# Kernel tuning notes

Measured on AMD Instinct MI355X. Metric: run time of the kernel, lower is better.

Reference implementation:

```python
import jax, jax.numpy as jnp
import numpy as np
from jax import lax

INV_SQRT2 = np.float32(1.0 / np.sqrt(2.0))

def conv2d(x, w, b=None, stride=1, pad=0):
    y = lax.conv_general_dilated(x, w, (stride, stride), [(pad, pad), (pad, pad)],
                                 dimension_numbers=('NCHW', 'OIHW', 'NCHW'))
    return y if b is None else y + b[None, :, None, None]

def haar_dwt2_zero(x):
    # pytorch_wavelets DWTForward(J=1, wave='haar', mode='zero') for odd H,W:
    # pad one zero at the end of each spatial dim, then pairwise Haar analysis.
    x = jnp.pad(x, ((0, 0), (0, 0), (0, 1), (0, 1)))
    xe, xo = x[..., 0::2], x[..., 1::2]
    lo_w, hi_w = (xe + xo) * INV_SQRT2, (xe - xo) * INV_SQRT2
    def rows(t):
        te, to = t[:, :, 0::2, :], t[:, :, 1::2, :]
        return (te + to) * INV_SQRT2, (te - to) * INV_SQRT2
    ll, lh = rows(lo_w)
    hl, hh = rows(hi_w)
    return ll, lh, hl, hh  # cA, cH, cV, cD

def pixel_shuffle2(x):
    B, C, H, W = x.shape
    co = C // 4
    return x.reshape(B, co, 2, 2, H, W).transpose(0, 1, 4, 2, 5, 3).reshape(B, co, H * 2, W * 2)

def gaussian_kernel5(sigma=0.5):
    r = np.arange(5, dtype=np.float64) - 2.0
    k = np.exp(-(r ** 2) / (2.0 * sigma * sigma))
    return jnp.asarray((k / k.sum()).astype(np.float32))

_GK = gaussian_kernel5(0.5)

def gaussian_blur5(x4d):
    # cv2.GaussianBlur ksize=(5,5) sigma=0.5, default BORDER_REFLECT_101 -> 'reflect' pad
    p = jnp.pad(x4d, ((0, 0), (0, 0), (2, 2), (2, 2)), mode='reflect')
    p = conv2d(p, _GK.reshape(1, 1, 5, 1))
    return conv2d(p, _GK.reshape(1, 1, 1, 5))

def channel_attention(x, w1, w2):
    avg = jnp.mean(x, axis=(2, 3), keepdims=True)
    mx = jnp.max(x, axis=(2, 3), keepdims=True)
    mlp = lambda v: conv2d(jax.nn.relu(conv2d(v, w1)), w2)
    return jax.nn.sigmoid(mlp(avg) + mlp(mx)) * x

def _forward(x, w_x1, b_x1, w_x2, b_x2, w_x3, b_x3, w_hi, b_hi, w_lo, b_lo,
             ca1_w1, ca1_w2, ca2_w1, ca2_w2, w_cat, b_cat, w_c9a, b_c9a, w_c9b, b_c9b):
    f1 = jax.nn.relu(conv2d(x, w_x1, b_x1))            # (1,16,H,W)
    f2 = jax.nn.relu(conv2d(f1, w_x2, b_x2))           # (1,8,H,W)
    tmp12 = jax.nn.relu(conv2d(f2, w_x3, b_x3))        # (1,1,H,W)
    cA, cH, cV, cD = haar_dwt2_zero(tmp12)             # each (1,1,(H+1)/2,(W+1)/2)
    hf = pixel_shuffle2(jax.nn.relu(conv2d(jnp.concatenate([cH, cV, cD], 1), w_hi, b_hi, pad=1)))
    lf = pixel_shuffle2(jax.nn.relu(conv2d(cA, w_lo, b_lo, pad=1)))  # (1,1,H+5,W+5)
    # original detaches hf (cpu->numpy->cv2->cuda): gradients do not flow through it
    hf = gaussian_blur5(lax.stop_gradient(hf))
    hf = channel_attention(hf, ca1_w1, ca1_w2)
    lf = channel_attention(lf, ca2_w1, ca2_w2)
    alpha = 1.0
    cat = jax.nn.relu(conv2d(jnp.concatenate([alpha * hf, (1.0 - alpha) * lf], 1), w_cat, b_cat))
    f12 = tmp12 + cat                                   # (1,1,H,W)
    h = jax.nn.relu(conv2d(f12, w_c9a, b_c9a, pad=1))   # (1,32,H,W)
    return jax.nn.relu(conv2d(h, w_c9b, b_c9b, pad=1))  # (1,64,H,W)

def setup_inputs() -> dict:
    key = jax.random.key(0)
    ks = jax.random.split(key, 24)
    f32 = jnp.float32
    n = lambda k, s, sc=0.05: jax.random.normal(k, s, f32) * sc
    H = W = 511
    return {
        'x': jax.random.normal(ks[0], (1, 204, H, W), f32),
        'w_x1': n(ks[1], (16, 204, 1, 1)), 'b_x1': n(ks[2], (16,)),
        'w_x2': n(ks[3], (8, 16, 1, 1)),   'b_x2': n(ks[4], (8,)),
        'w_x3': n(ks[5], (1, 8, 1, 1)),    'b_x3': n(ks[6], (1,)),
        'w_hi': n(ks[7], (4, 3, 1, 1)),    'b_hi': n(ks[8], (4,)),
        'w_lo': n(ks[9], (4, 1, 1, 1)),    'b_lo': n(ks[10], (4,)),
        'ca1_w1': n(ks[11], (1, 1, 1, 1), 0.5), 'ca1_w2': n(ks[12], (1, 1, 1, 1), 0.5),
        'ca2_w1': n(ks[13], (1, 1, 1, 1), 0.5), 'ca2_w2': n(ks[14], (1, 1, 1, 1), 0.5),
        'w_cat': n(ks[15], (1, 2, 6, 6)),  'b_cat': n(ks[16], (1,)),
        'w_c9a': n(ks[17], (32, 1, 3, 3)), 'b_c9a': n(ks[18], (32,)),
        'w_c9b': n(ks[19], (64, 32, 3, 3)), 'b_c9b': n(ks[20], (64,)),
    }

def reference(x, w_x1, b_x1, w_x2, b_x2, w_x3, b_x3, w_hi, b_hi, w_lo, b_lo,
              ca1_w1, ca1_w2, ca2_w1, ca2_w2, w_cat, b_cat, w_c9a, b_c9a, w_c9b, b_c9b):
    return _forward(x, w_x1, b_x1, w_x2, b_x2, w_x3, b_x3, w_hi, b_hi, w_lo, b_lo,
                    ca1_w1, ca1_w2, ca2_w1, ca2_w2, w_cat, b_cat, w_c9a, b_c9a, w_c9b, b_c9b)
```

## Files before the change

kernel.cpp:

```cpp
#include <hip/hip_runtime.h>
#include <hip/hip_bf16.h>
#include <math.h>

#define NP    261121
#define SPB   512
#define RS    520
#define OFS   16640
#define WPX   520
#define ROWN  4160
#define PSTR  2138240
#define NBP   289

typedef __attribute__((ext_vector_type(8))) short short8;
typedef __attribute__((ext_vector_type(4))) short short4v;
typedef __attribute__((ext_vector_type(4))) float f32x4;
typedef __attribute__((ext_vector_type(4), aligned(4))) float f32x4a;

static __device__ __forceinline__ unsigned short f2bf(float f) {
    unsigned int u = __builtin_bit_cast(unsigned int, f);
    u += 0x7FFFu + ((u >> 16) & 1u);
    return (unsigned short)(u >> 16);
}

static __device__ __forceinline__ short bf16s(float f) {
    __hip_bfloat16 h = __float2bfloat16(f);
    return __builtin_bit_cast(short, h);
}

__global__ __launch_bounds__(256, 2) void k_conv123(const float* __restrict__ x,
                                                    const float* __restrict__ w_x1,
                                                    const float* __restrict__ b1,
                                                    const float* __restrict__ w2,
                                                    const float* __restrict__ b2,
                                                    const float* __restrict__ w3,
                                                    const float* __restrict__ b3,
                                                    const float* __restrict__ w_c9b,
                                                    float* __restrict__ tmp12,
                                                    unsigned short* __restrict__ wb2,
                                                    unsigned short* __restrict__ h2)
{
    {
        int t = blockIdx.x * 256 + threadIdx.x;
        if (t < 18432) {
            int o = t / 288, ck = t - o * 288;
            int c = ck / 9, k = ck - c * 9;
            wb2[k * 2048 + o * 32 + c] = f2bf(w_c9b[t]);
        }
        short8 z8 = {0, 0, 0, 0, 0, 0, 0, 0};
        if (t < 4160) {
            int pl = t / 1040;
            int rr = t - pl * 1040;
            int row = rr >= 520 ? 512 : 0;
            int ch  = rr >= 520 ? rr - 520 : rr;
            *reinterpret_cast<short8*>(h2 + (size_t)pl * PSTR + (size_t)row * ROWN + ch * 8) = z8;
        }
        int z = t - 4160;
        if (z >= 0 && z < 6132) {
            int row = z / 12 + 1;
            int j = z - (row - 1) * 12;
            int pl = j / 3, cidx = j - pl * 3;
            int col = (cidx == 0) ? 0 : (cidx == 1 ? 512 : 513);
            *reinterpret_cast<short8*>(h2 + (size_t)pl * PSTR + (size_t)row * ROWN + col * 8) = z8;
        }
    }

    __shared__ unsigned short sb[2 * OFS];

    const int tid = threadIdx.x;
    const int v = tid >> 6, l = tid & 63;
    const int lpx = l & 15, kg = l >> 4;
    int pxb = blockIdx.x * SPB;
    if (pxb > NP - SPB) pxb = NP - SPB;

    short8 afr[7];
    {
        const float* wrow = w_x1 + lpx * 204;
#pragma unroll
        for (int ks = 0; ks < 7; ++ks)
#pragma unroll
            for (int j = 0; j < 8; ++j) {
                int c = ks * 32 + kg * 8 + j;
                afr[ks][j] = (short)f2bf(c < 204 ? wrow[c] : 0.f);
            }
    }

    const float* xb = x + pxb + 4 * l;
    const float* lpB[8];
#pragma unroll
    for (int i = 0; i < 8; ++i)
        lpB[i] = xb + (size_t)(v * 8 + i) * NP;

    f32x4 acc[8];
#pragma unroll
    for (int n = 0; n < 8; ++n) acc[n] = (f32x4){0.f, 0.f, 0.f, 0.f};

    f32x4a q0[8], q1[8];

#define LOADISSUE(KS) do { \
        _Pragma("unroll") \
        for (int i = 0; i < 8; ++i) { \
            const float* p = ((KS) < 6 || v * 8 + i < 12) ? lpB[i] + (size_t)(KS) * 32 * NP : xb; \
            q0[i] = *reinterpret_cast<const f32x4a*>(p); \
            q1[i] = *reinterpret_cast<const f32x4a*>(p + 256); \
        } \
    } while (0)

#define CVTWRITE(BUF) do { \
        _Pragma("unroll") \
        for (int i = 0; i < 8; ++i) { \
            unsigned short* row = sb + (BUF) * OFS + (v * 8 + i) * RS; \
            short4v w0, w1; \
            _Pragma("unroll") \
            for (int n = 0; n < 4; ++n) { w0[n] = bf16s(q0[i][n]); w1[n] = bf16s(q1[i][n]); } \
            *reinterpret_cast<short4v*>(row + 4 * l)       = w0; \
            *reinterpret_cast<short4v*>(row + 256 + 4 * l) = w1; \
        } \
    } while (0)

#define COMPUTE(KS, BUF) do { \
        short8 r0, r1, r2, r3, r4, r5, r6, r7; \
        const unsigned short* base = sb + (BUF) * OFS + kg * 8 * RS + v * 128 + lpx * 8; \
        r0 = *reinterpret_cast<const short8*>(base); \
        r1 = *reinterpret_cast<const short8*>(base + RS); \
        r2 = *reinterpret_cast<const short8*>(base + 2 * RS); \
        r3 = *reinterpret_cast<const short8*>(base + 3 * RS); \
        r4 = *reinterpret_cast<const short8*>(base + 4 * RS); \
        r5 = *reinterpret_cast<const short8*>(base + 5 * RS); \
        r6 = *reinterpret_cast<const short8*>(base + 6 * RS); \
        r7 = *reinterpret_cast<const short8*>(base + 7 * RS); \
        _Pragma("unroll") \
        for (int n = 0; n < 8; ++n) { \
            short8 b; \
            b[0] = r0[n]; b[1] = r1[n]; b[2] = r2[n]; b[3] = r3[n]; \
            b[4] = r4[n]; b[5] = r5[n]; b[6] = r6[n]; b[7] = r7[n]; \
            acc[n] = __builtin_amdgcn_mfma_f32_16x16x32_bf16(afr[KS], b, acc[n], 0, 0, 0); \
        } \
    } while (0)

    LOADISSUE(0);
    CVTWRITE(0);

#define STEP(K, LAST) do { \
        if (!(LAST)) LOADISSUE((K) + 1); \
        __syncthreads(); \
        COMPUTE((K), (K) & 1); \
        if (!(LAST)) CVTWRITE(((K) + 1) & 1); \
    } while (0)

    STEP(0, 0); STEP(1, 0); STEP(2, 0); STEP(3, 0); STEP(4, 0); STEP(5, 0); STEP(6, 1);
#undef LOADISSUE
#undef CVTWRITE
#undef COMPUTE
#undef STEP

    float4 b1v = *reinterpret_cast<const float4*>(b1 + kg * 4);
    float4 w2v[8];
#pragma unroll
    for (int j = 0; j < 8; ++j)
        w2v[j] = *reinterpret_cast<const float4*>(w2 + j * 16 + kg * 4);
    float b2v[8], w3v[8];
#pragma unroll
    for (int j = 0; j < 8; ++j) { b2v[j] = b2[j]; w3v[j] = w3[j]; }
    float b3v = b3[0];

    f32x4 rlo, rhi;
#pragma unroll
    for (int n = 0; n < 8; ++n) {
        float f0 = fmaxf(acc[n][0] + b1v.x, 0.f);
        float f1 = fmaxf(acc[n][1] + b1v.y, 0.f);
        float f2 = fmaxf(acc[n][2] + b1v.z, 0.f);
        float f3 = fmaxf(acc[n][3] + b1v.w, 0.f);
        float tmp = b3v;
#pragma unroll
        for (int j = 0; j < 8; ++j) {
            float sj = f0 * w2v[j].x;
            sj = fmaf(f1, w2v[j].y, sj);
            sj = fmaf(f2, w2v[j].z, sj);
            sj = fmaf(f3, w2v[j].w, sj);
            sj += __shfl_xor(sj, 16, 64);
            sj += __shfl_xor(sj, 32, 64);
            tmp = fmaf(fmaxf(sj + b2v[j], 0.f), w3v[j], tmp);
        }
        if (n < 4) rlo[n] = fmaxf(tmp, 0.f);
        else       rhi[n - 4] = fmaxf(tmp, 0.f);
    }
    if (kg == 0) {
        float* dst = tmp12 + pxb + v * 128 + lpx * 8;
        *reinterpret_cast<f32x4a*>(dst)     = rlo;
        *reinterpret_cast<f32x4a*>(dst + 4) = rhi;
    }
}

__global__ __launch_bounds__(256) void k_dwtblur(const float* __restrict__ tmp12,
                                                 const float* __restrict__ w_hi,
                                                 const float* __restrict__ b_hi,
                                                 float* __restrict__ hfb,
                                                 float* __restrict__ psum,
                                                 float* __restrict__ pmax,
                                                 float g0, float g1, float g2)
{
    __shared__ float hfT[36][37];
    __shared__ float ss[256], sm[256];
    const float INV = 0.70710678118654752440f;

    int tid = threadIdx.x;
    int bx = blockIdx.x % 17, by = blockIdx.x / 17;
    int X0 = bx * 32, Y0 = by * 32;
    int Ylo = Y0 - 2 < 0 ? 0 : Y0 - 2;
    int Yhi = Y0 + 33 > 515 ? 515 : Y0 + 33;
    int Xlo = X0 - 2 < 0 ? 0 : X0 - 2;
    int Xhi = X0 + 33 > 515 ? 515 : X0 + 33;
    int hlo = Ylo >> 1, hhi = Yhi >> 1, nh = hhi - hlo + 1;
    int wlo = Xlo >> 1, whi = Xhi >> 1, nw = whi - wlo + 1;
    int ncells = nh * nw;

    float wh[12], bh[4];
#pragma unroll
    for (int i = 0; i < 12; ++i) wh[i] = w_hi[i];
#pragma unroll
    for (int o = 0; o < 4; ++o) bh[o] = b_hi[o];

    for (int ci = tid; ci < ncells; ci += 256) {
        int h = hlo + ci / nw, w = wlo + ci % nw;
        float v[4];
        if (h == 0 || h == 257 || w == 0 || w == 257) {
#pragma unroll
            for (int o = 0; o < 4; ++o) v[o] = fmaxf(bh[o], 0.f);
        } else {
            int hh = h - 1, ww = w - 1;
            int r0 = 2 * hh, r1 = 2 * hh + 1, c0 = 2 * ww, c1 = 2 * ww + 1;
            float a = tmp12[r0 * 511 + c0];
            float b = (c1 < 511) ? tmp12[r0 * 511 + c1] : 0.f;
            float c = (r1 < 511) ? tmp12[r1 * 511 + c0] : 0.f;
            float d = (r1 < 511 && c1 < 511) ? tmp12[r1 * 511 + c1] : 0.f;
            float lo0 = (a + b) * INV, hi0 = (a - b) * INV;
            float lo1 = (c + d) * INV, hi1 = (c - d) * INV;
            float cH = (lo0 - lo1) * INV;
            float cV = (hi0 + hi1) * INV;
            float cD = (hi0 - hi1) * INV;
#pragma unroll
            for (int o = 0; o < 4; ++o)
                v[o] = fmaxf(wh[o * 3 + 0] * cH + wh[o * 3 + 1] * cV + wh[o * 3 + 2] * cD + bh[o], 0.f);
        }
#pragma unroll
        for (int dy = 0; dy < 2; ++dy)
#pragma unroll
            for (int dx = 0; dx < 2; ++dx) {
                int Y = 2 * h + dy, X = 2 * w + dx;
                if (Y >= Ylo && Y <= Yhi && X >= Xlo && X <= Xhi)
                    hfT[Y - Y0 + 2][X - X0 + 2] = v[dy * 2 + dx];
            }
    }
    __syncthreads();

    float g[5] = {g0, g1, g2, g1, g0};
    float lsum = 0.f, lmax = -3.4e38f;
#pragma unroll
    for (int k2 = 0; k2 < 4; ++k2) {
        int o = tid + k2 * 256;
        int oy = o >> 5, ox = o & 31;
        int gy = Y0 + oy, gx = X0 + ox;
        if (gy < 516 && gx < 516) {
            int ly[5], lx[5];
#pragma unroll
            for (int i = 0; i < 5; ++i) {
                int yy = gy + i - 2; yy = yy < 0 ? -yy : (yy > 515 ? 1030 - yy : yy);
                int xx = gx + i - 2; xx = xx < 0 ? -xx : (xx > 515 ? 1030 - xx : xx);
                ly[i] = yy - Y0 + 2; lx[i] = xx - X0 + 2;
            }
            float s = 0.f;
#pragma unroll
            for (int i = 0; i < 5; ++i) {
                float rs = 0.f;
#pragma unroll
                for (int j = 0; j < 5; ++j) rs = fmaf(g[j], hfT[ly[i]][lx[j]], rs);
                s = fmaf(g[i], rs, s);
            }
            hfb[gy * 516 + gx] = s;
            lsum += s; lmax = fmaxf(lmax, s);
        }
    }

    ss[tid] = lsum; sm[tid] = lmax;
    __syncthreads();
    for (int off = 128; off > 0; off >>= 1) {
        if (tid < off) { ss[tid] += ss[tid + off]; sm[tid] = fmaxf(sm[tid], sm[tid + off]); }
        __syncthreads();
    }
    if (tid == 0) { psum[blockIdx.x] = ss[0]; pmax[blockIdx.x] = sm[0]; }
}

__global__ __launch_bounds__(256) void k_catc9a(const float* __restrict__ hfb,
                                                const float* __restrict__ tmp12,
                                                const float* __restrict__ psum,
                                                const float* __restrict__ pmax,
                                                const float* __restrict__ caw1,
                                                const float* __restrict__ caw2,
                                                const float* __restrict__ w_cat,
                                                const float* __restrict__ b_cat,
                                                const float* __restrict__ w_c9a,
                                                const float* __restrict__ bias9a,
                                                unsigned short* __restrict__ h2)
{
    __shared__ float f12T[18][19];
    __shared__ float ss[256], sm[256];
    __shared__ float ssc;
    int tid = threadIdx.x;

    {
        float s = 0.f, m = -3.4e38f;
        for (int i = tid; i < NBP; i += 256) { s += psum[i]; m = fmaxf(m, pmax[i]); }
        ss[tid] = s; sm[tid] = m;
        __syncthreads();
        for (int off = 128; off > 0; off >>= 1) {
            if (tid < off) { ss[tid] += ss[tid + off]; sm[tid] = fmaxf(sm[tid], sm[tid + off]); }
            __syncthreads();
        }
        if (tid == 0) {
            float avg = ss[0] / 266256.f;
            float a = caw1[0], b = caw2[0];
            float z = b * fmaxf(a * avg, 0.f) + b * fmaxf(a * sm[0], 0.f);
            ssc = 1.f / (1.f + expf(-z));
        }
        __syncthreads();
    }
    float sc = ssc;

    int tx0 = (blockIdx.x & 31) * 16, ty0 = (blockIdx.x >> 5) * 16;

    for (int idx = tid; idx < 324; idx += 256) {
        int r = idx / 18, c = idx - 18 * r;
        int fy = ty0 - 1 + r, fx = tx0 - 1 + c;
        float val = 0.f;
        if (fy >= 0 && fy < 511 && fx >= 0 && fx < 511) {
            float a6 = 0.f;
#pragma unroll
            for (int ky = 0; ky < 6; ++ky) {
                const float* row = hfb + (fy + ky) * 516 + fx;
#pragma unroll
                for (int kx = 0; kx < 6; ++kx) a6 = fmaf(row[kx], w_cat[ky * 6 + kx], a6);
            }
            val = tmp12[fy * 511 + fx] + fmaxf(sc * a6 + b_cat[0], 0.f);
        }
        f12T[r][c] = val;
    }
    __syncthreads();

    int lr = tid >> 4, lc = tid & 15;
    int oy = ty0 + lr, ox = tx0 + lc;
    if (oy >= 511 || ox >= 511) return;

    float hv[9];
#pragma unroll
    for (int ky = 0; ky < 3; ++ky)
#pragma unroll
        for (int kx = 0; kx < 3; ++kx)
            hv[ky * 3 + kx] = f12T[lr + ky][lc + kx];

    float acc[32];
#pragma unroll
    for (int o = 0; o < 32; ++o) acc[o] = bias9a[o];
#pragma unroll
    for (int k = 0; k < 9; ++k) {
        float v = hv[k];
#pragma unroll
        for (int o = 0; o < 32; ++o) acc[o] = fmaf(v, w_c9a[o * 9 + k], acc[o]);
    }
    unsigned short o16[32];
#pragma unroll
    for (int o = 0; o < 32; ++o) o16[o] = f2bf(fmaxf(acc[o], 0.f));
    size_t px = (size_t)(oy + 1) * WPX + (ox + 1);
#pragma unroll
    for (int i = 0; i < 4; ++i)
        *reinterpret_cast<short8*>(h2 + (size_t)i * PSTR + px * 8) =
            reinterpret_cast<const short8*>(o16)[i];
}

__global__ __launch_bounds__(256, 3) void k_c9b(const unsigned short* __restrict__ h2,
                                                const unsigned short* __restrict__ wb2,
                                                const float* __restrict__ bias,
                                                float* __restrict__ out)
{
    __shared__ unsigned short swu[9 * 2048];

    int bid = blockIdx.x;
    int xcd = bid & 7, jj = bid >> 3;
    const int q = 127, r = 6;
    int wg = (xcd < r ? xcd * (q + 1) : r * (q + 1) + (xcd - r) * q) + jj;

    int lane = threadIdx.x & 63;
    int wave = threadIdx.x >> 6;
    int y  = wg >> 1;
    int xh = wg & 1;
    int xb = xh * 256 + wave * 64;
    int lpx = lane & 15, kg = lane >> 4;

    {
        const short8* wsrc = reinterpret_cast<const short8*>(wb2);
        short8* wdst = reinterpret_cast<short8*>(swu);
        for (int d = threadIdx.x; d < 2304; d += 256) {
            int kt = d >> 8, rem = d & 255, m = rem >> 6, l = rem & 63;
            wdst[d] = wsrc[kt * 256 + (m * 16 + (l & 15)) * 4 + (l >> 4)];
        }
    }
    __syncthreads();

    f32x4 acc[4][4];
#pragma unroll
    for (int m = 0; m < 4; ++m)
#pragma unroll
        for (int n = 0; n < 4; ++n) acc[m][n] = (f32x4){0.f, 0.f, 0.f, 0.f};

    const unsigned short* hb = h2 + (size_t)kg * PSTR;
    const int base_px = (y + 1) * WPX + (xb + 1) + lpx;
    const int rowm = base_px - WPX, row0 = base_px, rowp = base_px + WPX;
    const short8* swv = reinterpret_cast<const short8*>(swu);

#define LOADB(BUF, ROW, DX) do { \
        const unsigned short* rp = hb + (size_t)((ROW) + (DX)) * 8; \
        BUF[0] = *reinterpret_cast<const short8*>(rp); \
        BUF[1] = *reinterpret_cast<const short8*>(rp + 128); \
        BUF[2] = *reinterpret_cast<const short8*>(rp + 256); \
        BUF[3] = *reinterpret_cast<const short8*>(rp + 384); \
    } while (0)

#define TAP(KT, BUF) do { \
        const short8* ap = swv + (KT) * 256 + lane; \
        short8 a0 = ap[0], a1 = ap[64], a2 = ap[128], a3 = ap[192]; \
        _Pragma("unroll") \
        for (int n = 0; n < 4; ++n) { \
            acc[0][n] = __builtin_amdgcn_mfma_f32_16x16x32_bf16(a0, BUF[n], acc[0][n], 0, 0, 0); \
            acc[1][n] = __builtin_amdgcn_mfma_f32_16x16x32_bf16(a1, BUF[n], acc[1][n], 0, 0, 0); \
            acc[2][n] = __builtin_amdgcn_mfma_f32_16x16x32_bf16(a2, BUF[n], acc[2][n], 0, 0, 0); \
            acc[3][n] = __builtin_amdgcn_mfma_f32_16x16x32_bf16(a3, BUF[n], acc[3][n], 0, 0, 0); \
        } \
    } while (0)

    short8 bX[4], bY[4], bZ[4];
    LOADB(bX, rowm, -1);
    LOADB(bY, rowm,  0);
    LOADB(bZ, rowm, +1); TAP(0, bX);
    LOADB(bX, row0, -1); TAP(1, bY);
    LOADB(bY, row0,  0); TAP(2, bZ);
    LOADB(bZ, row0, +1); TAP(3, bX);
    LOADB(bX, rowp, -1); TAP(4, bY);
    LOADB(bY, rowp,  0); TAP(5, bZ);
    LOADB(bZ, rowp, +1); TAP(6, bX);
    TAP(7, bY);
    TAP(8, bZ);
#undef LOADB
#undef TAP

    const int ybase = y * 511;
#pragma unroll
    for (int m = 0; m < 4; ++m) {
#pragma unroll
        for (int rr = 0; rr < 4; ++rr) {
            int o = m * 16 + kg * 4 + rr;
            float bo = bias[o];
#pragma unroll
            for (int n = 0; n < 4; ++n) {
                int px = xb + n * 16 + lpx;
                if (px < 511)
                    out[(size_t)o * NP + ybase + px] = fmaxf(acc[m][n][rr] + bo, 0.f);
            }
        }
    }
}

extern "C" void kernel_launch(void* const* d_in, const int* in_sizes, int n_in,
                              void* d_out, int out_size, void* d_ws, size_t ws_size,
                              hipStream_t stream)
{
    (void)in_sizes; (void)n_in; (void)out_size; (void)ws_size;

    const float* x     = (const float*)d_in[0];
    const float* w_x1  = (const float*)d_in[1];
    const float* b_x1  = (const float*)d_in[2];
    const float* w_x2  = (const float*)d_in[3];
    const float* b_x2  = (const float*)d_in[4];
    const float* w_x3  = (const float*)d_in[5];
    const float* b_x3  = (const float*)d_in[6];
    const float* w_hi  = (const float*)d_in[7];
    const float* b_hi  = (const float*)d_in[8];
    const float* ca1w1 = (const float*)d_in[11];
    const float* ca1w2 = (const float*)d_in[12];
    const float* w_cat = (const float*)d_in[15];
    const float* b_cat = (const float*)d_in[16];
    const float* w_c9a = (const float*)d_in[17];
    const float* b_c9a = (const float*)d_in[18];
    const float* w_c9b = (const float*)d_in[19];
    const float* b_c9b = (const float*)d_in[20];

    float* ws    = (float*)d_ws;
    float* tmp12 = ws + 0;
    float* hfb   = ws + 261184;
    float* psum  = ws + 527488;
    float* pmax  = ws + 527808;
    unsigned short* wb2 = (unsigned short*)(ws + 528128);
    unsigned short* h2  = (unsigned short*)(ws + 537344);

    float* out = (float*)d_out;

    double kk[5], ssum = 0.0;
    for (int i = 0; i < 5; ++i) { double r = i - 2.0; kk[i] = exp(-r * r / 0.5); ssum += kk[i]; }
    float g0 = (float)(kk[0] / ssum), g1 = (float)(kk[1] / ssum), g2 = (float)(kk[2] / ssum);

    k_conv123<<<511, 256, 0, stream>>>(x, w_x1, b_x1, w_x2, b_x2, w_x3, b_x3, w_c9b,
                                       tmp12, wb2, h2);
    k_dwtblur<<<NBP, 256, 0, stream>>>(tmp12, w_hi, b_hi, hfb, psum, pmax, g0, g1, g2);
    k_catc9a<<<1024, 256, 0, stream>>>(hfb, tmp12, psum, pmax, ca1w1, ca1w2,
                                       w_cat, b_cat, w_c9a, b_c9a, h2);
    k_c9b<<<1022, 256, 0, stream>>>(h2, wb2, b_c9b, out);
}
```

Baseline: 103.4 us.

## Halve conv123 tile, stage fp32 in LDS with aligned loads, convert at compute

The first conv kernel now handles 256 pixels per block instead of 512 and launches 1021 blocks instead of 511. Input rows are staged into LDS as fp32 using 16-byte-aligned global loads with a per-row shift fix-up, replacing unaligned 4-byte-aligned vector loads. The bf16 conversion moves from the staging step to the MFMA operand build. The register-held prefetch across the barrier is gone: loads go straight to the other LDS buffer after the barrier. This aims to improve load coalescing and occupancy for the bandwidth-bound 204-channel read, but it loses explicit register prefetch overlap and doubles LDS bytes per pixel.

```diff
diff --git a/kernel.cpp b/kernel.cpp
--- a/kernel.cpp
+++ b/kernel.cpp
@@ -3,16 +3,15 @@
 #include <math.h>
 
 #define NP    261121
-#define SPB   512
-#define RS    520
-#define OFS   16640
+#define SPB   256
+#define RSF   264
+#define OFSF  8448
 #define WPX   520
 #define ROWN  4160
 #define PSTR  2138240
 #define NBP   289
 
 typedef __attribute__((ext_vector_type(8))) short short8;
-typedef __attribute__((ext_vector_type(4))) short short4v;
 typedef __attribute__((ext_vector_type(4))) float f32x4;
 typedef __attribute__((ext_vector_type(4), aligned(4))) float f32x4a;
 
@@ -64,7 +63,7 @@
         }
     }
 
-    __shared__ unsigned short sb[2 * OFS];
+    __shared__ float sb[2 * OFSF];
 
     const int tid = threadIdx.x;
     const int v = tid >> 6, l = tid & 63;
@@ -84,72 +83,58 @@
             }
     }
 
-    const float* xb = x + pxb + 4 * l;
-    const float* lpB[8];
-#pragma unroll
-    for (int i = 0; i < 8; ++i)
-        lpB[i] = xb + (size_t)(v * 8 + i) * NP;
-
-    f32x4 acc[8];
-#pragma unroll
-    for (int n = 0; n < 8; ++n) acc[n] = (f32x4){0.f, 0.f, 0.f, 0.f};
-
-    f32x4a q0[8], q1[8];
-
-#define LOADISSUE(KS) do { \
+    f32x4 acc[4];
+#pragma unroll
+    for (int n = 0; n < 4; ++n) acc[n] = (f32x4){0.f, 0.f, 0.f, 0.f};
+
+#define STAGE(KS) do { \
         _Pragma("unroll") \
         for (int i = 0; i < 8; ++i) { \
-            const float* p = ((KS) < 6 || v * 8 + i < 12) ? lpB[i] + (size_t)(KS) * 32 * NP : xb; \
-            q0[i] = *reinterpret_cast<const f32x4a*>(p); \
-            q1[i] = *reinterpret_cast<const f32x4a*>(p + 256); \
+            const int ch = v * 8 + i; \
+            const int cc = ((KS) < 6 || ch < 12) ? ((KS) * 32 + ch) : 0; \
+            const size_t g = (size_t)cc * NP + pxb; \
+            const int s = (int)(g & 3); \
+            const f32x4* ap = reinterpret_cast<const f32x4*>(x + (g - s)); \
+            f32x4 m = ap[l];                        \
+            float* row = sb + ((KS) & 1) * OFSF + ch * RSF; \
+            *reinterpret_cast<f32x4a*>(row + 4 + 4 * l - s) = m; \
+            if (s && l == 0) {                      \
+                f32x4 tl = ap[64]; \
+                *reinterpret_cast<f32x4a*>(row + 4 + 256 - s) = tl; \
+            } \
         } \
     } while (0)
 
-#define CVTWRITE(BUF) do { \
+#define COMPUTE(KS) do { \
+        const float* base = sb + ((KS) & 1) * OFSF + (kg * 8) * RSF + 4 + v * 64 + lpx * 4; \
+        f32x4 r0 = *reinterpret_cast<const f32x4*>(base); \
+        f32x4 r1 = *reinterpret_cast<const f32x4*>(base + RSF); \
+        f32x4 r2 = *reinterpret_cast<const f32x4*>(base + 2 * RSF); \
+        f32x4 r3 = *reinterpret_cast<const f32x4*>(base + 3 * RSF); \
+        f32x4 r4 = *reinterpret_cast<const f32x4*>(base + 4 * RSF); \
+        f32x4 r5 = *reinterpret_cast<const f32x4*>(base + 5 * RSF); \
+        f32x4 r6 = *reinterpret_cast<const f32x4*>(base + 6 * RSF); \
+        f32x4 r7 = *reinterpret_cast<const f32x4*>(base + 7 * RSF); \
         _Pragma("unroll") \
-        for (int i = 0; i < 8; ++i) { \
-            unsigned short* row = sb + (BUF) * OFS + (v * 8 + i) * RS; \
-            short4v w0, w1; \
-            _Pragma("unroll") \
-            for (int n = 0; n < 4; ++n) { w0[n] = bf16s(q0[i][n]); w1[n] = bf16s(q1[i][n]); } \
-            *reinterpret_cast<short4v*>(row + 4 * l)       = w0; \
-            *reinterpret_cast<short4v*>(row + 256 + 4 * l) = w1; \
-        } \
-    } while (0)
-
-#define COMPUTE(KS, BUF) do { \
-        short8 r0, r1, r2, r3, r4, r5, r6, r7; \
-        const unsigned short* base = sb + (BUF) * OFS + kg * 8 * RS + v * 128 + lpx * 8; \
-        r0 = *reinterpret_cast<const short8*>(base); \
-        r1 = *reinterpret_cast<const short8*>(base + RS); \
-        r2 = *reinterpret_cast<const short8*>(base + 2 * RS); \
-        r3 = *reinterpret_cast<const short8*>(base + 3 * RS); \
-        r4 = *reinterpret_cast<const short8*>(base + 4 * RS); \
-        r5 = *reinterpret_cast<const short8*>(base + 5 * RS); \
-        r6 = *reinterpret_cast<const short8*>(base + 6 * RS); \
-        r7 = *reinterpret_cast<const short8*>(base + 7 * RS); \
-        _Pragma("unroll") \
-        for (int n = 0; n < 8; ++n) { \
+        for (int n = 0; n < 4; ++n) { \
             short8 b; \
-            b[0] = r0[n]; b[1] = r1[n]; b[2] = r2[n]; b[3] = r3[n]; \
-            b[4] = r4[n]; b[5] = r5[n]; b[6] = r6[n]; b[7] = r7[n]; \
+            b[0] = bf16s(r0[n]); b[1] = bf16s(r1[n]); \
+            b[2] = bf16s(r2[n]); b[3] = bf16s(r3[n]); \
+            b[4] = bf16s(r4[n]); b[5] = bf16s(r5[n]); \
+            b[6] = bf16s(r6[n]); b[7] = bf16s(r7[n]); \
             acc[n] = __builtin_amdgcn_mfma_f32_16x16x32_bf16(afr[KS], b, acc[n], 0, 0, 0); \
         } \
     } while (0)
 
-    LOADISSUE(0);
-    CVTWRITE(0);
-
+    STAGE(0);
 #define STEP(K, LAST) do { \
-        if (!(LAST)) LOADISSUE((K) + 1); \
         __syncthreads(); \
-        COMPUTE((K), (K) & 1); \
-        if (!(LAST)) CVTWRITE(((K) + 1) & 1); \
+        if (!(LAST)) STAGE((K) + 1); \
+        COMPUTE(K); \
     } while (0)
 
     STEP(0, 0); STEP(1, 0); STEP(2, 0); STEP(3, 0); STEP(4, 0); STEP(5, 0); STEP(6, 1);
-#undef LOADISSUE
-#undef CVTWRITE
+#undef STAGE
 #undef COMPUTE
 #undef STEP
 
@@ -163,9 +148,9 @@
     for (int j = 0; j < 8; ++j) { b2v[j] = b2[j]; w3v[j] = w3[j]; }
     float b3v = b3[0];
 
-    f32x4 rlo, rhi;
-#pragma unroll
-    for (int n = 0; n < 8; ++n) {
+    f32x4 resv;
+#pragma unroll
+    for (int n = 0; n < 4; ++n) {
         float f0 = fmaxf(acc[n][0] + b1v.x, 0.f);
         float f1 = fmaxf(acc[n][1] + b1v.y, 0.f);
         float f2 = fmaxf(acc[n][2] + b1v.z, 0.f);
@@ -181,14 +166,10 @@
             sj += __shfl_xor(sj, 32, 64);
             tmp = fmaf(fmaxf(sj + b2v[j], 0.f), w3v[j], tmp);
         }
-        if (n < 4) rlo[n] = fmaxf(tmp, 0.f);
-        else       rhi[n - 4] = fmaxf(tmp, 0.f);
-    }
-    if (kg == 0) {
-        float* dst = tmp12 + pxb + v * 128 + lpx * 8;
-        *reinterpret_cast<f32x4a*>(dst)     = rlo;
-        *reinterpret_cast<f32x4a*>(dst + 4) = rhi;
-    }
+        resv[n] = fmaxf(tmp, 0.f);
+    }
+    if (kg == 0)
+        *reinterpret_cast<f32x4a*>(tmp12 + pxb + v * 64 + lpx * 4) = resv;
 }
 
 __global__ __launch_bounds__(256) void k_dwtblur(const float* __restrict__ tmp12,
@@ -506,8 +487,8 @@
     for (int i = 0; i < 5; ++i) { double r = i - 2.0; kk[i] = exp(-r * r / 0.5); ssum += kk[i]; }
     float g0 = (float)(kk[0] / ssum), g1 = (float)(kk[1] / ssum), g2 = (float)(kk[2] / ssum);
 
-    k_conv123<<<511, 256, 0, stream>>>(x, w_x1, b_x1, w_x2, b_x2, w_x3, b_x3, w_c9b,
-                                       tmp12, wb2, h2);
+    k_conv123<<<1021, 256, 0, stream>>>(x, w_x1, b_x1, w_x2, b_x2, w_x3, b_x3, w_c9b,
+                                        tmp12, wb2, h2);
     k_dwtblur<<<NBP, 256, 0, stream>>>(tmp12, w_hi, b_hi, hfb, psum, pmax, g0, g1, g2);
     k_catc9a<<<1024, 256, 0, stream>>>(hfb, tmp12, psum, pmax, ca1w1, ca1w2,
                                        w_cat, b_cat, w_c9a, b_c9a, h2);
```

After: 153.8 us. 48.7% more time.
